# Kernel tuning notes

Measured on AMD Instinct MI355X. Metric: run time of the kernel, lower is better.

Reference implementation:

```python
import jax, jax.numpy as jnp
import numpy as np

# ---- problem dims ----
B, S, C, H, W = 4, 8, 3, 256, 256
P = 68          # keypoints (self.points)
DS = 4          # detector downsample
WIN = 8
STEPS = 10      # Gauss-Newton iterations per frame pair
EPS = 1e-6
GRAY_W = jnp.array([0.299, 0.587, 0.114], dtype=jnp.float32)

# window offsets [K,2] in (x,y)
_rng = jnp.arange(-WIN, WIN + 1, dtype=jnp.float32)
_OFF = jnp.stack(jnp.meshgrid(_rng, _rng, indexing='xy'), -1).reshape(-1, 2)


def setup_inputs() -> dict:
    key = jax.random.key(0)
    k1, k2 = jax.random.split(key)
    inputs = jax.random.normal(k1, (B, S, C, H, W), dtype=jnp.float32)
    Wdet = jax.random.normal(k2, (P, C, 3, 3), dtype=jnp.float32) * 0.1
    bdet = jnp.zeros((P,), dtype=jnp.float32)
    return {"inputs": inputs, "Wdet": Wdet, "bdet": bdet}


def _bilinear(img, xy):
    # img [H,W]; xy [...,2] in (x,y) pixel coords -> sampled values [...]
    x = jnp.clip(xy[..., 0], 0.0, W - 1.001)
    y = jnp.clip(xy[..., 1], 0.0, H - 1.001)
    x0 = jnp.floor(x); y0 = jnp.floor(y)
    wx = x - x0; wy = y - y0
    x0i = x0.astype(jnp.int32); y0i = y0.astype(jnp.int32)
    x1i = jnp.minimum(x0i + 1, W - 1); y1i = jnp.minimum(y0i + 1, H - 1)
    v00 = img[y0i, x0i]; v01 = img[y0i, x1i]
    v10 = img[y1i, x0i]; v11 = img[y1i, x1i]
    return (1 - wy) * ((1 - wx) * v00 + wx * v01) + wy * ((1 - wx) * v10 + wx * v11)


def _grad_xy(img):
    # central differences with edge replication
    px = jnp.pad(img, ((0, 0), (1, 1)), mode='edge')
    py = jnp.pad(img, ((1, 1), (0, 0)), mode='edge')
    gx = (px[:, 2:] - px[:, :-2]) * 0.5
    gy = (py[2:, :] - py[:-2, :]) * 0.5
    return gx, gy


def _lk_track(old, new, pts):
    # one Lucas-Kanade tracking step: old/new [H,W] gray, pts [P,2] -> [P,2]
    gx, gy = _grad_xy(old)
    pos0 = pts[:, None, :] + _OFF[None]            # [P,K,2]
    I0 = _bilinear(old, pos0)                      # [P,K] template patch
    Ix = _bilinear(gx, pos0)
    Iy = _bilinear(gy, pos0)
    Gxx = (Ix * Ix).sum(-1); Gxy = (Ix * Iy).sum(-1); Gyy = (Iy * Iy).sum(-1)
    det = Gxx * Gyy - Gxy * Gxy + EPS
    Ginv = jnp.stack([jnp.stack([Gyy, -Gxy], -1),
                      jnp.stack([-Gxy, Gxx], -1)], -2) / det[:, None, None]  # [P,2,2]

    def step(i, v):
        I1 = _bilinear(new, pos0 + v[:, None, :])  # [P,K]
        err = I0 - I1
        b = jnp.stack([(err * Ix).sum(-1), (err * Iy).sum(-1)], -1)  # [P,2]
        return v + jnp.einsum('pij,pj->pi', Ginv, b)

    v = jax.lax.fori_loop(0, STEPS, step, jnp.zeros_like(pts))
    return pts + v


def _lk_forward_backward(gray, locs):
    # gray [S,H,W], locs [S,P,2] -> nextPts, fbackPts, backPts each [S,P,2]
    def f(pts, frames):
        o, n = frames
        q = _lk_track(o, n, pts)
        return q, q

    # forward: track detector locs of frame 0 through the sequence
    _, fout = jax.lax.scan(f, locs[0], (gray[:-1], gray[1:]))
    nextPts = jnp.concatenate([locs[:1], fout], 0)
    ro, rn = gray[1:][::-1], gray[:-1][::-1]
    # forward-backward: track the forward end point back to frame 0
    _, fbout = jax.lax.scan(f, nextPts[-1], (ro, rn))
    fbackPts = jnp.concatenate([nextPts[-1:], fbout], 0)[::-1]
    # backward: track detector locs of last frame back through the sequence
    _, bout = jax.lax.scan(f, locs[-1], (ro, rn))
    backPts = jnp.concatenate([locs[-1:], bout], 0)[::-1]
    return nextPts, fbackPts, backPts


def _detector(x, Wdet, bdet):
    # x [N,C,H,W] -> heatmaps [N,P,H/DS,W/DS], locs [N,P,2] (pixel coords), scores [N,P]
    hm = jax.lax.conv_general_dilated(
        x, Wdet, window_strides=(DS, DS), padding='SAME',
        dimension_numbers=('NCHW', 'OIHW', 'NCHW')) + bdet[None, :, None, None]
    N, _, Hd, Wd = hm.shape
    flat = hm.reshape(N, P, Hd * Wd)
    prob = jax.nn.softmax(flat, axis=-1)
    ys, xs = jnp.meshgrid(jnp.arange(Hd, dtype=hm.dtype),
                          jnp.arange(Wd, dtype=hm.dtype), indexing='ij')
    ex = (prob * xs.reshape(-1)).sum(-1) * DS   # soft-argmax, upscaled to input px
    ey = (prob * ys.reshape(-1)).sum(-1) * DS
    locs = jnp.stack([ex, ey], -1)
    scos = flat.max(-1)
    return hm, locs, scos


def reference(inputs, Wdet, bdet):
    x = inputs.reshape(B * S, C, H, W)
    hm, locs, scos = _detector(x, Wdet, bdet)
    heatmaps = hm.reshape(B, S, P, H // DS, W // DS)
    batch_locs = locs.reshape(B, S, P, 2)
    batch_scos = scos.reshape(B, S, P)
    gray = jnp.einsum('bschw,c->bshw', inputs, GRAY_W)  # [B,S,H,W]
    nextPts, fbackPts, backPts = jax.vmap(_lk_forward_backward)(gray, batch_locs)
    return heatmaps, batch_locs, batch_scos, nextPts, fbackPts, backPts
```

## Files before the change

### kernel.cpp

```cpp
#include <hip/hip_runtime.h>
#include <math.h>

namespace {
constexpr int Bn = 4, Sn = 8, Cn = 3, Himg = 256, Wimg = 256;
constexpr int Pn = 68, DS = 4, WIN = 8, STEPS = 10;
constexpr int HWi = Himg * Wimg;
constexpr int NIMG = Bn * Sn;
constexpr int HD = Himg / DS, WD = Wimg / DS;
constexpr int Kwin = (2 * WIN + 1) * (2 * WIN + 1);
}

__global__ __launch_bounds__(256) void gray2_kernel(const float* __restrict__ in,
                                                    float* __restrict__ gray,
                                                    float* __restrict__ sh) {
    int idx = blockIdx.x * blockDim.x + threadIdx.x;
    int total = NIMG * HWi / 4;
    if (idx >= total) return;
    int img = idx / (HWi / 4);
    int off = idx % (HWi / 4);
    const float* base = in + (size_t)img * 3 * HWi;
    float4 c0 = ((const float4*)(base))[off];
    float4 c1 = ((const float4*)(base + HWi))[off];
    float4 c2 = ((const float4*)(base + 2 * HWi))[off];
    float4 g;
    g.x = 0.299f * c0.x + 0.587f * c1.x + 0.114f * c2.x;
    g.y = 0.299f * c0.y + 0.587f * c1.y + 0.114f * c2.y;
    g.z = 0.299f * c0.z + 0.587f * c1.z + 0.114f * c2.z;
    g.w = 0.299f * c0.w + 0.587f * c1.w + 0.114f * c2.w;
    float gn = 0.f;
    int gi = idx * 4 + 4;
    if (gi < NIMG * HWi) {
        int i2 = gi / HWi;
        int o2 = gi % HWi;
        const float* b2 = in + (size_t)i2 * 3 * HWi;
        gn = 0.299f * b2[o2] + 0.587f * b2[o2 + HWi] + 0.114f * b2[o2 + 2 * HWi];
    }
    ((float4*)(gray + (size_t)img * HWi))[off] = g;
    float4 s;
    s.x = g.y; s.y = g.z; s.z = g.w; s.w = gn;
    ((float4*)(sh + (size_t)img * HWi))[off] = s;
}

__global__ __launch_bounds__(256) void conv_kernel(const float* __restrict__ x,
                                                   const float* __restrict__ Wdet,
                                                   const float* __restrict__ bdet,
                                                   float* __restrict__ hm) {
    __shared__ float wsh[Pn * 27];
    __shared__ float bsh[Pn];
    __shared__ float insh[3][3][Wimg];
    int n = blockIdx.x >> 6;
    int oy = blockIdx.x & 63;
    int tid = threadIdx.x;
    for (int t = tid; t < Pn * 27; t += 256) wsh[t] = Wdet[t];
    if (tid < Pn) bsh[tid] = bdet[tid];
    for (int t = tid; t < 3 * 3 * Wimg; t += 256) {
        int c = t / (3 * Wimg);
        int r = (t / Wimg) % 3;
        int col = t % Wimg;
        insh[c][r][col] = x[(size_t)n * 3 * HWi + (size_t)c * HWi + (oy * 4 + r) * Wimg + col];
    }
    __syncthreads();
    int ox = tid & 63;
    int wid = tid >> 6;
    float in_reg[27];
    #pragma unroll
    for (int c = 0; c < 3; c++)
        #pragma unroll
        for (int ky = 0; ky < 3; ky++)
            #pragma unroll
            for (int kx = 0; kx < 3; kx++)
                in_reg[c * 9 + ky * 3 + kx] = insh[c][ky][ox * 4 + kx];
    #pragma unroll
    for (int i = 0; i < 17; i++) {
        int p = wid + i * 4;
        const float* w = &wsh[p * 27];
        float acc = bsh[p];
        #pragma unroll
        for (int j = 0; j < 27; j++) acc += w[j] * in_reg[j];
        hm[(size_t)n * Pn * 4096 + (size_t)p * 4096 + oy * 64 + ox] = acc;
    }
}

__global__ __launch_bounds__(256) void smax_kernel(const float* __restrict__ hm,
                                                   float* __restrict__ locs,
                                                   float* __restrict__ scos) {
    int row = blockIdx.x;
    const float4* r = (const float4*)(hm + (size_t)row * 4096);
    int tid = threadIdx.x;
    float v[16];
    #pragma unroll
    for (int j = 0; j < 4; j++) {
        float4 q = r[tid + 256 * j];
        v[4 * j + 0] = q.x; v[4 * j + 1] = q.y; v[4 * j + 2] = q.z; v[4 * j + 3] = q.w;
    }
    float m = v[0];
    #pragma unroll
    for (int i = 1; i < 16; i++) m = fmaxf(m, v[i]);
    __shared__ float redm[4];
    #pragma unroll
    for (int o = 32; o; o >>= 1) m = fmaxf(m, __shfl_xor(m, o, 64));
    int wid = tid >> 6, lane = tid & 63;
    if (lane == 0) redm[wid] = m;
    __syncthreads();
    m = fmaxf(fmaxf(redm[0], redm[1]), fmaxf(redm[2], redm[3]));
    float s = 0.f, sx = 0.f, sy = 0.f;
    #pragma unroll
    for (int j = 0; j < 4; j++) {
        #pragma unroll
        for (int q = 0; q < 4; q++) {
            int e = (tid + 256 * j) * 4 + q;
            float ev = expf(v[4 * j + q] - m);
            s += ev;
            sx += ev * (float)(e & 63);
            sy += ev * (float)(e >> 6);
        }
    }
    #pragma unroll
    for (int o = 32; o; o >>= 1) {
        s  += __shfl_xor(s, o, 64);
        sx += __shfl_xor(sx, o, 64);
        sy += __shfl_xor(sy, o, 64);
    }
    __shared__ float reds[3][4];
    if (lane == 0) { reds[0][wid] = s; reds[1][wid] = sx; reds[2][wid] = sy; }
    __syncthreads();
    if (tid == 0) {
        float S_ = reds[0][0] + reds[0][1] + reds[0][2] + reds[0][3];
        float SX = reds[1][0] + reds[1][1] + reds[1][2] + reds[1][3];
        float SY = reds[2][0] + reds[2][1] + reds[2][2] + reds[2][3];
        locs[(size_t)row * 2 + 0] = SX / S_ * 4.0f;
        locs[(size_t)row * 2 + 1] = SY / S_ * 4.0f;
        scos[row] = m;
    }
}

template <int CTRL>
__device__ inline float dpp_add(float v) {
    int t = __builtin_amdgcn_update_dpp(0, __builtin_bit_cast(int, v), CTRL, 0xF, 0xF, true);
    return v + __builtin_bit_cast(float, t);
}

__device__ inline float wredw(float v) {
    v = dpp_add<0x111>(v);
    v = dpp_add<0x112>(v);
    v = dpp_add<0x114>(v);
    v = dpp_add<0x118>(v);
    v = dpp_add<0x142>(v);
    v = dpp_add<0x143>(v);
    int s = __builtin_amdgcn_readlane(__builtin_bit_cast(int, v), 63);
    return __builtin_bit_cast(float, s);
}

__device__ void lk_track_pair(const float* __restrict__ oldI, const float* __restrict__ oldS,
                              const float* __restrict__ newI, const float* __restrict__ newS,
                              float& px, float& py, const float* dxs, const float* dys,
                              float s4w) {
    const float XM = (float)(Wimg - 1.001);
    const float YM = (float)(Himg - 1.001);
    float I0[5], Ix[5], Iy[5], qx[5], qy[5];
    {
        float wx[5], wy[5];
        const float* pb[5];
        int xe[5], am[5], a0[5], a1[5], ap[5], xm[5], xp[5];
        #pragma unroll
        for (int j = 0; j < 5; j++) {
            qx[j] = px + dxs[j];
            qy[j] = py + dys[j];
            float x = fminf(fmaxf(qx[j], 0.0f), XM);
            float y = fminf(fmaxf(qy[j], 0.0f), YM);
            float x0f = floorf(x), y0f = floorf(y);
            wx[j] = x - x0f; wy[j] = y - y0f;
            int xi = (int)x0f, yi = (int)y0f;
            xe[j] = xi & ~1;
            pb[j] = (xi & 1) ? oldS : oldI;
            xm[j] = max(xi - 1, 0);
            xp[j] = min(xi + 2, Wimg - 1);
            a0[j] = yi * Wimg;
            a1[j] = a0[j] + Wimg;
            am[j] = max(yi - 1, 0) * Wimg;
            ap[j] = min(yi + 2, Himg - 1) * Wimg;
        }
        float2 Pm[5], P0[5], P1[5], Pp[5];
        float c0m[5], c0p[5], c1m[5], c1p[5];
        #pragma unroll
        for (int j = 0; j < 5; j++) {
            Pm[j] = *(const float2*)(pb[j] + am[j] + xe[j]);
            P0[j] = *(const float2*)(pb[j] + a0[j] + xe[j]);
            P1[j] = *(const float2*)(pb[j] + a1[j] + xe[j]);
            Pp[j] = *(const float2*)(pb[j] + ap[j] + xe[j]);
            c0m[j] = oldI[a0[j] + xm[j]];
            c0p[j] = oldI[a0[j] + xp[j]];
            c1m[j] = oldI[a1[j] + xm[j]];
            c1p[j] = oldI[a1[j] + xp[j]];
        }
        #pragma unroll
        for (int j = 0; j < 5; j++) {
            float m0 = Pm[j].x, m1 = Pm[j].y;
            float c00 = P0[j].x, c01 = P0[j].y;
            float c10 = P1[j].x, c11 = P1[j].y;
            float p0 = Pp[j].x, p1 = Pp[j].y;
            float u = 1.0f - wx[j], t = 1.0f - wy[j];
            I0[j] = t * (u * c00 + wx[j] * c01) + wy[j] * (u * c10 + wx[j] * c11);
            float gx00 = 0.5f * (c01 - c0m[j]);
            float gx01 = 0.5f * (c0p[j] - c00);
            float gx10 = 0.5f * (c11 - c1m[j]);
            float gx11 = 0.5f * (c1p[j] - c10);
            Ix[j] = t * (u * gx00 + wx[j] * gx01) + wy[j] * (u * gx10 + wx[j] * gx11);
            float gy00 = 0.5f * (c10 - m0);
            float gy01 = 0.5f * (c11 - m1);
            float gy10 = 0.5f * (p0 - c00);
            float gy11 = 0.5f * (p1 - c01);
            Iy[j] = t * (u * gy00 + wx[j] * gy01) + wy[j] * (u * gy10 + wx[j] * gy11);
        }
        Ix[4] *= s4w;
        Iy[4] *= s4w;
    }
    float gxx = 0.f, gxy = 0.f, gyy = 0.f;
    #pragma unroll
    for (int j = 0; j < 5; j++) { gxx += Ix[j] * Ix[j]; gxy += Ix[j] * Iy[j]; gyy += Iy[j] * Iy[j]; }
    gxx = wredw(gxx); gxy = wredw(gxy); gyy = wredw(gyy);
    float det = gxx * gyy - gxy * gxy + 1e-6f;
    float A = gyy / det, Bv = -gxy / det, D = gxx / det;
    float vx = 0.f, vy = 0.f;
    for (int it = 0; it < STEPS; ++it) {
        float fx[5], fy[5];
        const float* pb[5];
        int aa[5];
        #pragma unroll
        for (int j = 0; j < 5; j++) {
            float x = fminf(fmaxf(qx[j] + vx, 0.0f), XM);
            float y = fminf(fmaxf(qy[j] + vy, 0.0f), YM);
            float x0f = floorf(x), y0f = floorf(y);
            fx[j] = x - x0f; fy[j] = y - y0f;
            int xi = (int)x0f, yi = (int)y0f;
            pb[j] = (xi & 1) ? newS : newI;
            aa[j] = yi * Wimg + (xi & ~1);
        }
        float2 R0[5], R1[5];
        #pragma unroll
        for (int j = 0; j < 5; j++) {
            R0[j] = *(const float2*)(pb[j] + aa[j]);
            R1[j] = *(const float2*)(pb[j] + aa[j] + Wimg);
        }
        float bx = 0.f, by = 0.f;
        #pragma unroll
        for (int j = 0; j < 5; j++) {
            float u = 1.0f - fx[j], t = 1.0f - fy[j];
            float I1 = t * (u * R0[j].x + fx[j] * R0[j].y) + fy[j] * (u * R1[j].x + fx[j] * R1[j].y);
            float err = I0[j] - I1;
            bx += err * Ix[j];
            by += err * Iy[j];
        }
        bx = wredw(bx); by = wredw(by);
        vx += A * bx + Bv * by;
        vy += Bv * bx + D * by;
    }
    px += vx; py += vy;
}

__global__ __launch_bounds__(64) void lk_pair_kernel(const float* __restrict__ gray,
                                                     const float* __restrict__ sh,
                                                     const float* __restrict__ locs,
                                                     float* __restrict__ nextPts,
                                                     float* __restrict__ fbackPts,
                                                     float* __restrict__ backPts) {
    int g = blockIdx.x;
    int typ = g / (Bn * Pn);
    int r = g % (Bn * Pn);
    int b = r / Pn;
    int p = r % Pn;
    int lane = threadIdx.x;
    const float* G = gray + (size_t)b * Sn * HWi;
    const float* S = sh + (size_t)b * Sn * HWi;
    float dxs[5], dys[5];
    #pragma unroll
    for (int j = 0; j < 4; j++) {
        int k = lane + 64 * j;
        dxs[j] = (float)(k % 17 - 8);
        dys[j] = (float)(k / 17 - 8);
    }
    {
        int k4 = (lane < Kwin - 256) ? 256 + lane : 256;
        dxs[4] = (float)(k4 % 17 - 8);
        dys[4] = (float)(k4 / 17 - 8);
    }
    float s4w = (lane < Kwin - 256) ? 1.0f : 0.0f;
    auto LIDX = [&](int s) { return (((size_t)b * Sn + s) * Pn + p) * 2; };
    if (typ == 0) {
        float px = locs[LIDX(0)], py = locs[LIDX(0) + 1];
        if (lane == 0) { nextPts[LIDX(0)] = px; nextPts[LIDX(0) + 1] = py; }
        for (int s = 0; s < 7; s++) {
            lk_track_pair(G + s * HWi, S + s * HWi, G + (s + 1) * HWi, S + (s + 1) * HWi,
                          px, py, dxs, dys, s4w);
            if (lane == 0) { nextPts[LIDX(s + 1)] = px; nextPts[LIDX(s + 1) + 1] = py; }
        }
        if (lane == 0) { fbackPts[LIDX(7)] = px; fbackPts[LIDX(7) + 1] = py; }
        for (int i = 0; i < 7; i++) {
            lk_track_pair(G + (7 - i) * HWi, S + (7 - i) * HWi, G + (6 - i) * HWi, S + (6 - i) * HWi,
                          px, py, dxs, dys, s4w);
            if (lane == 0) { fbackPts[LIDX(6 - i)] = px; fbackPts[LIDX(6 - i) + 1] = py; }
        }
    } else {
        float px = locs[LIDX(7)], py = locs[LIDX(7) + 1];
        if (lane == 0) { backPts[LIDX(7)] = px; backPts[LIDX(7) + 1] = py; }
        for (int i = 0; i < 7; i++) {
            lk_track_pair(G + (7 - i) * HWi, S + (7 - i) * HWi, G + (6 - i) * HWi, S + (6 - i) * HWi,
                          px, py, dxs, dys, s4w);
            if (lane == 0) { backPts[LIDX(6 - i)] = px; backPts[LIDX(6 - i) + 1] = py; }
        }
    }
}

__device__ inline float px_fly(const float* __restrict__ im, int idx) {
    return 0.299f * im[idx] + 0.587f * im[idx + HWi] + 0.114f * im[idx + 2 * HWi];
}

__device__ void lk_track_fly(const float* __restrict__ oldI, const float* __restrict__ newI,
                             float& px, float& py, const float* dxs, const float* dys,
                             float s4w) {
    const float XM = (float)(Wimg - 1.001);
    const float YM = (float)(Himg - 1.001);
    float I0[5], Ix[5], Iy[5], qx[5], qy[5];
    {
        float wx[5], wy[5];
        int am[5], a0[5], a1[5], ap[5], xm[5], x0[5], x1[5], xp[5];
        #pragma unroll
        for (int j = 0; j < 5; j++) {
            qx[j] = px + dxs[j]; qy[j] = py + dys[j];
            float x = fminf(fmaxf(qx[j], 0.0f), XM);
            float y = fminf(fmaxf(qy[j], 0.0f), YM);
            float x0f = floorf(x), y0f = floorf(y);
            wx[j] = x - x0f; wy[j] = y - y0f;
            int xi = (int)x0f, yi = (int)y0f;
            x0[j] = xi; x1[j] = min(xi + 1, Wimg - 1);
            xm[j] = max(xi - 1, 0); xp[j] = min(xi + 2, Wimg - 1);
            a0[j] = yi * Wimg;
            a1[j] = min(yi + 1, Himg - 1) * Wimg;
            am[j] = max(yi - 1, 0) * Wimg;
            ap[j] = min(yi + 2, Himg - 1) * Wimg;
        }
        #pragma unroll
        for (int j = 0; j < 5; j++) {
            float m0 = px_fly(oldI, am[j] + x0[j]), m1 = px_fly(oldI, am[j] + x1[j]);
            float c0m = px_fly(oldI, a0[j] + xm[j]), c00 = px_fly(oldI, a0[j] + x0[j]);
            float c01 = px_fly(oldI, a0[j] + x1[j]), c0p = px_fly(oldI, a0[j] + xp[j]);
            float c1m = px_fly(oldI, a1[j] + xm[j]), c10 = px_fly(oldI, a1[j] + x0[j]);
            float c11 = px_fly(oldI, a1[j] + x1[j]), c1p = px_fly(oldI, a1[j] + xp[j]);
            float p0 = px_fly(oldI, ap[j] + x0[j]), p1 = px_fly(oldI, ap[j] + x1[j]);
            float u = 1.0f - wx[j], t = 1.0f - wy[j];
            I0[j] = t * (u * c00 + wx[j] * c01) + wy[j] * (u * c10 + wx[j] * c11);
            Ix[j] = t * (u * 0.5f * (c01 - c0m) + wx[j] * 0.5f * (c0p - c00))
                  + wy[j] * (u * 0.5f * (c11 - c1m) + wx[j] * 0.5f * (c1p - c10));
            Iy[j] = t * (u * 0.5f * (c10 - m0) + wx[j] * 0.5f * (c11 - m1))
                  + wy[j] * (u * 0.5f * (p0 - c00) + wx[j] * 0.5f * (p1 - c01));
        }
        Ix[4] *= s4w; Iy[4] *= s4w;
    }
    float gxx = 0.f, gxy = 0.f, gyy = 0.f;
    #pragma unroll
    for (int j = 0; j < 5; j++) { gxx += Ix[j] * Ix[j]; gxy += Ix[j] * Iy[j]; gyy += Iy[j] * Iy[j]; }
    gxx = wredw(gxx); gxy = wredw(gxy); gyy = wredw(gyy);
    float det = gxx * gyy - gxy * gxy + 1e-6f;
    float A = gyy / det, Bv = -gxy / det, D = gxx / det;
    float vx = 0.f, vy = 0.f;
    for (int it = 0; it < STEPS; ++it) {
        float bx = 0.f, by = 0.f;
        #pragma unroll
        for (int j = 0; j < 5; j++) {
            float x = fminf(fmaxf(qx[j] + vx, 0.0f), XM);
            float y = fminf(fmaxf(qy[j] + vy, 0.0f), YM);
            float x0f = floorf(x), y0f = floorf(y);
            float fxx = x - x0f, fyy = y - y0f;
            int xi = (int)x0f, yi = (int)y0f;
            int ad = yi * Wimg + xi;
            float v00 = px_fly(newI, ad), v01 = px_fly(newI, ad + 1);
            float v10 = px_fly(newI, ad + Wimg), v11 = px_fly(newI, ad + Wimg + 1);
            float u = 1.0f - fxx, t = 1.0f - fyy;
            float I1 = t * (u * v00 + fxx * v01) + fyy * (u * v10 + fxx * v11);
            float err = I0[j] - I1;
            bx += err * Ix[j];
            by += err * Iy[j];
        }
        bx = wredw(bx); by = wredw(by);
        vx += A * bx + Bv * by;
        vy += Bv * bx + D * by;
    }
    px += vx; py += vy;
}

__global__ __launch_bounds__(64) void lk_fly_kernel(const float* __restrict__ in,
                                                    const float* __restrict__ locs,
                                                    float* __restrict__ nextPts,
                                                    float* __restrict__ fbackPts,
                                                    float* __restrict__ backPts) {
    constexpr size_t FS = (size_t)3 * HWi;
    int g = blockIdx.x;
    int typ = g / (Bn * Pn);
    int r = g % (Bn * Pn);
    int b = r / Pn;
    int p = r % Pn;
    int lane = threadIdx.x;
    const float* G = in + (size_t)b * Sn * FS;
    float dxs[5], dys[5];
    #pragma unroll
    for (int j = 0; j < 4; j++) {
        int k = lane + 64 * j;
        dxs[j] = (float)(k % 17 - 8);
        dys[j] = (float)(k / 17 - 8);
    }
    {
        int k4 = (lane < Kwin - 256) ? 256 + lane : 256;
        dxs[4] = (float)(k4 % 17 - 8);
        dys[4] = (float)(k4 / 17 - 8);
    }
    float s4w = (lane < Kwin - 256) ? 1.0f : 0.0f;
    auto LIDX = [&](int s) { return (((size_t)b * Sn + s) * Pn + p) * 2; };
    if (typ == 0) {
        float px = locs[LIDX(0)], py = locs[LIDX(0) + 1];
        if (lane == 0) { nextPts[LIDX(0)] = px; nextPts[LIDX(0) + 1] = py; }
        for (int s = 0; s < 7; s++) {
            lk_track_fly(G + s * FS, G + (s + 1) * FS, px, py, dxs, dys, s4w);
            if (lane == 0) { nextPts[LIDX(s + 1)] = px; nextPts[LIDX(s + 1) + 1] = py; }
        }
        if (lane == 0) { fbackPts[LIDX(7)] = px; fbackPts[LIDX(7) + 1] = py; }
        for (int i = 0; i < 7; i++) {
            lk_track_fly(G + (7 - i) * FS, G + (6 - i) * FS, px, py, dxs, dys, s4w);
            if (lane == 0) { fbackPts[LIDX(6 - i)] = px; fbackPts[LIDX(6 - i) + 1] = py; }
        }
    } else {
        float px = locs[LIDX(7)], py = locs[LIDX(7) + 1];
        if (lane == 0) { backPts[LIDX(7)] = px; backPts[LIDX(7) + 1] = py; }
        for (int i = 0; i < 7; i++) {
            lk_track_fly(G + (7 - i) * FS, G + (6 - i) * FS, px, py, dxs, dys, s4w);
            if (lane == 0) { backPts[LIDX(6 - i)] = px; backPts[LIDX(6 - i) + 1] = py; }
        }
    }
}

extern "C" void kernel_launch(void* const* d_in, const int* in_sizes, int n_in,
                              void* d_out, int out_size, void* d_ws, size_t ws_size,
                              hipStream_t stream) {
    const float* inputs = (const float*)d_in[0];
    const float* Wdet = (const float*)d_in[1];
    const float* bdet = (const float*)d_in[2];
    float* out = (float*)d_out;

    const size_t N_hm = (size_t)Bn * Sn * Pn * HD * WD;
    const size_t N_pts = (size_t)Bn * Sn * Pn * 2;
    float* hm = out;
    float* locs = out + N_hm;
    float* scos = locs + N_pts;
    float* nextPts = scos + (size_t)Bn * Sn * Pn;
    float* fbackPts = nextPts + N_pts;
    float* backPts = fbackPts + N_pts;

    conv_kernel<<<NIMG * 64, 256, 0, stream>>>(inputs, Wdet, bdet, hm);
    smax_kernel<<<NIMG * Pn, 256, 0, stream>>>(hm, locs, scos);

    const size_t gray_elems = (size_t)NIMG * HWi;
    if (ws_size >= 2 * gray_elems * sizeof(float)) {
        float* gray = (float*)d_ws;
        float* sh = gray + gray_elems;
        gray2_kernel<<<(NIMG * HWi / 4 + 255) / 256, 256, 0, stream>>>(inputs, gray, sh);
        lk_pair_kernel<<<2 * Bn * Pn, 64, 0, stream>>>(gray, sh, locs, nextPts, fbackPts, backPts);
    } else {
        lk_fly_kernel<<<2 * Bn * Pn, 64, 0, stream>>>(inputs, locs, nextPts, fbackPts, backPts);
    }
}
```

Baseline: 121.7 us.

## Fuse grayscale into conv kernel and store quad-packed float4 bilinear layout

Removes the separate gray conversion kernel by computing grayscale rows inside the convolution kernel from the shared-memory input tile. The kernel writes a quad layout where each float4 holds the 2x2 bilinear neighbourhood, so each LK sample is one 16-byte load instead of two float2 loads chosen by parity. The first iteration reuses the template-time fetch of the new frame. This costs a larger workspace (4x the gray size) and more write traffic from the conv kernel, and the fly fallback gains edge-clamp fixes.

```diff
diff --git a/kernel.cpp b/kernel.cpp
--- a/kernel.cpp
+++ b/kernel.cpp
@@ -8,37 +8,76 @@
 constexpr int NIMG = Bn * Sn;
 constexpr int HD = Himg / DS, WD = Wimg / DS;
 constexpr int Kwin = (2 * WIN + 1) * (2 * WIN + 1);
-}
-
-__global__ __launch_bounds__(256) void gray2_kernel(const float* __restrict__ in,
-                                                    float* __restrict__ gray,
-                                                    float* __restrict__ sh) {
-    int idx = blockIdx.x * blockDim.x + threadIdx.x;
-    int total = NIMG * HWi / 4;
-    if (idx >= total) return;
-    int img = idx / (HWi / 4);
-    int off = idx % (HWi / 4);
-    const float* base = in + (size_t)img * 3 * HWi;
-    float4 c0 = ((const float4*)(base))[off];
-    float4 c1 = ((const float4*)(base + HWi))[off];
-    float4 c2 = ((const float4*)(base + 2 * HWi))[off];
-    float4 g;
-    g.x = 0.299f * c0.x + 0.587f * c1.x + 0.114f * c2.x;
-    g.y = 0.299f * c0.y + 0.587f * c1.y + 0.114f * c2.y;
-    g.z = 0.299f * c0.z + 0.587f * c1.z + 0.114f * c2.z;
-    g.w = 0.299f * c0.w + 0.587f * c1.w + 0.114f * c2.w;
-    float gn = 0.f;
-    int gi = idx * 4 + 4;
-    if (gi < NIMG * HWi) {
-        int i2 = gi / HWi;
-        int o2 = gi % HWi;
-        const float* b2 = in + (size_t)i2 * 3 * HWi;
-        gn = 0.299f * b2[o2] + 0.587f * b2[o2 + HWi] + 0.114f * b2[o2 + 2 * HWi];
-    }
-    ((float4*)(gray + (size_t)img * HWi))[off] = g;
-    float4 s;
-    s.x = g.y; s.y = g.z; s.z = g.w; s.w = gn;
-    ((float4*)(sh + (size_t)img * HWi))[off] = s;
+constexpr int QROWS = 257;
+constexpr int QFR = QROWS * 256;
+}
+
+__global__ __launch_bounds__(256) void mega_kernel(const float* __restrict__ x,
+                                                   const float* __restrict__ Wdet,
+                                                   const float* __restrict__ bdet,
+                                                   float* __restrict__ hm,
+                                                   float4* __restrict__ Q) {
+    __shared__ float wsh[Pn * 27];
+    __shared__ float bsh[Pn];
+    __shared__ float insh[3][5][Wimg];
+    __shared__ float grow[5][257];
+    int n = blockIdx.x >> 6;
+    int oy = blockIdx.x & 63;
+    int tid = threadIdx.x;
+    for (int t = tid; t < Pn * 27; t += 256) wsh[t] = Wdet[t];
+    if (tid < Pn) bsh[tid] = bdet[tid];
+    for (int t = tid; t < 3 * 5 * Wimg; t += 256) {
+        int c = t / (5 * Wimg);
+        int rem = t % (5 * Wimg);
+        int r = rem / Wimg;
+        int col = rem % Wimg;
+        int gr = min(max(4 * oy - 1 + r, 0), 255);
+        insh[c][r][col] = x[(size_t)n * 3 * HWi + (size_t)c * HWi + gr * Wimg + col];
+    }
+    __syncthreads();
+    int ox = tid & 63;
+    int wid = tid >> 6;
+    float in_reg[27];
+    #pragma unroll
+    for (int c = 0; c < 3; c++)
+        #pragma unroll
+        for (int ky = 0; ky < 3; ky++)
+            #pragma unroll
+            for (int kx = 0; kx < 3; kx++)
+                in_reg[c * 9 + ky * 3 + kx] = insh[c][1 + ky][ox * 4 + kx];
+    #pragma unroll
+    for (int i = 0; i < 17; i++) {
+        int p = wid + i * 4;
+        const float* w = &wsh[p * 27];
+        float acc = bsh[p];
+        #pragma unroll
+        for (int j = 0; j < 27; j++) acc += w[j] * in_reg[j];
+        hm[(size_t)n * Pn * 4096 + (size_t)p * 4096 + oy * 64 + ox] = acc;
+    }
+    #pragma unroll
+    for (int r = 0; r < 5; r++)
+        grow[r][tid] = 0.299f * insh[0][r][tid] + 0.587f * insh[1][r][tid] + 0.114f * insh[2][r][tid];
+    if (tid < 5) grow[tid][256] = grow[tid][255];
+    __syncthreads();
+    float4* qf = Q + (size_t)n * QFR;
+    #pragma unroll
+    for (int j = 0; j < 4; j++) {
+        int k = 4 * oy + j;
+        float4 q;
+        q.x = grow[j][tid];
+        q.y = grow[j + 1][tid];
+        q.z = grow[j][tid + 1];
+        q.w = grow[j + 1][tid + 1];
+        qf[k * 256 + tid] = q;
+    }
+    if (oy == 63) {
+        float4 q;
+        q.x = grow[4][tid];
+        q.y = grow[4][tid];
+        q.z = grow[4][tid + 1];
+        q.w = grow[4][tid + 1];
+        qf[256 * 256 + tid] = q;
+    }
 }
 
 __global__ __launch_bounds__(256) void conv_kernel(const float* __restrict__ x,
@@ -151,60 +190,51 @@
     return __builtin_bit_cast(float, s);
 }
 
-__device__ void lk_track_pair(const float* __restrict__ oldI, const float* __restrict__ oldS,
-                              const float* __restrict__ newI, const float* __restrict__ newS,
-                              float& px, float& py, const float* dxs, const float* dys,
-                              float s4w) {
+__device__ void lk_track_q(const float4* __restrict__ Qo, const float4* __restrict__ Qn,
+                           float& px, float& py, const float* dxs, const float* dys,
+                           float s4w) {
     const float XM = (float)(Wimg - 1.001);
     const float YM = (float)(Himg - 1.001);
     float I0[5], Ix[5], Iy[5], qx[5], qy[5];
+    float wx[5], wy[5];
+    float4 Q0[5];
     {
-        float wx[5], wy[5];
-        const float* pb[5];
-        int xe[5], am[5], a0[5], a1[5], ap[5], xm[5], xp[5];
+        int idA[5], idS[5], xm[5], xp[5];
         #pragma unroll
         for (int j = 0; j < 5; j++) {
             qx[j] = px + dxs[j];
             qy[j] = py + dys[j];
             float x = fminf(fmaxf(qx[j], 0.0f), XM);
             float y = fminf(fmaxf(qy[j], 0.0f), YM);
-            float x0f = floorf(x), y0f = floorf(y);
-            wx[j] = x - x0f; wy[j] = y - y0f;
-            int xi = (int)x0f, yi = (int)y0f;
-            xe[j] = xi & ~1;
-            pb[j] = (xi & 1) ? oldS : oldI;
+            float xf = floorf(x), yf = floorf(y);
+            wx[j] = x - xf; wy[j] = y - yf;
+            int xi = (int)xf, yi = (int)yf;
+            idA[j] = yi * 256 + xi;
+            idS[j] = (yi + 1) * 256;
             xm[j] = max(xi - 1, 0);
             xp[j] = min(xi + 2, Wimg - 1);
-            a0[j] = yi * Wimg;
-            a1[j] = a0[j] + Wimg;
-            am[j] = max(yi - 1, 0) * Wimg;
-            ap[j] = min(yi + 2, Himg - 1) * Wimg;
-        }
-        float2 Pm[5], P0[5], P1[5], Pp[5];
-        float c0m[5], c0p[5], c1m[5], c1p[5];
-        #pragma unroll
-        for (int j = 0; j < 5; j++) {
-            Pm[j] = *(const float2*)(pb[j] + am[j] + xe[j]);
-            P0[j] = *(const float2*)(pb[j] + a0[j] + xe[j]);
-            P1[j] = *(const float2*)(pb[j] + a1[j] + xe[j]);
-            Pp[j] = *(const float2*)(pb[j] + ap[j] + xe[j]);
-            c0m[j] = oldI[a0[j] + xm[j]];
-            c0p[j] = oldI[a0[j] + xp[j]];
-            c1m[j] = oldI[a1[j] + xm[j]];
-            c1p[j] = oldI[a1[j] + xp[j]];
-        }
-        #pragma unroll
-        for (int j = 0; j < 5; j++) {
-            float m0 = Pm[j].x, m1 = Pm[j].y;
-            float c00 = P0[j].x, c01 = P0[j].y;
-            float c10 = P1[j].x, c11 = P1[j].y;
-            float p0 = Pp[j].x, p1 = Pp[j].y;
+        }
+        float4 A[5], B[5];
+        float2 S1[5], S2[5];
+        #pragma unroll
+        for (int j = 0; j < 5; j++) {
+            A[j] = Qo[idA[j]];
+            B[j] = Qo[idA[j] + 512];
+            S1[j] = *reinterpret_cast<const float2*>(Qo + idS[j] + xm[j]);
+            S2[j] = *reinterpret_cast<const float2*>(Qo + idS[j] + xp[j]);
+            Q0[j] = Qn[idA[j] + 256];
+        }
+        #pragma unroll
+        for (int j = 0; j < 5; j++) {
+            float m0 = A[j].x, c00 = A[j].y, m1 = A[j].z, c01 = A[j].w;
+            float c10 = B[j].x, p0 = B[j].y, c11 = B[j].z, p1 = B[j].w;
+            float c0m = S1[j].x, c1m = S1[j].y, c0p = S2[j].x, c1p = S2[j].y;
             float u = 1.0f - wx[j], t = 1.0f - wy[j];
             I0[j] = t * (u * c00 + wx[j] * c01) + wy[j] * (u * c10 + wx[j] * c11);
-            float gx00 = 0.5f * (c01 - c0m[j]);
-            float gx01 = 0.5f * (c0p[j] - c00);
-            float gx10 = 0.5f * (c11 - c1m[j]);
-            float gx11 = 0.5f * (c1p[j] - c10);
+            float gx00 = 0.5f * (c01 - c0m);
+            float gx01 = 0.5f * (c0p - c00);
+            float gx10 = 0.5f * (c11 - c1m);
+            float gx11 = 0.5f * (c1p - c10);
             Ix[j] = t * (u * gx00 + wx[j] * gx01) + wy[j] * (u * gx10 + wx[j] * gx11);
             float gy00 = 0.5f * (c10 - m0);
             float gy01 = 0.5f * (c11 - m1);
@@ -222,31 +252,12 @@
     float det = gxx * gyy - gxy * gxy + 1e-6f;
     float A = gyy / det, Bv = -gxy / det, D = gxx / det;
     float vx = 0.f, vy = 0.f;
-    for (int it = 0; it < STEPS; ++it) {
-        float fx[5], fy[5];
-        const float* pb[5];
-        int aa[5];
-        #pragma unroll
-        for (int j = 0; j < 5; j++) {
-            float x = fminf(fmaxf(qx[j] + vx, 0.0f), XM);
-            float y = fminf(fmaxf(qy[j] + vy, 0.0f), YM);
-            float x0f = floorf(x), y0f = floorf(y);
-            fx[j] = x - x0f; fy[j] = y - y0f;
-            int xi = (int)x0f, yi = (int)y0f;
-            pb[j] = (xi & 1) ? newS : newI;
-            aa[j] = yi * Wimg + (xi & ~1);
-        }
-        float2 R0[5], R1[5];
-        #pragma unroll
-        for (int j = 0; j < 5; j++) {
-            R0[j] = *(const float2*)(pb[j] + aa[j]);
-            R1[j] = *(const float2*)(pb[j] + aa[j] + Wimg);
-        }
+    {
         float bx = 0.f, by = 0.f;
         #pragma unroll
         for (int j = 0; j < 5; j++) {
-            float u = 1.0f - fx[j], t = 1.0f - fy[j];
-            float I1 = t * (u * R0[j].x + fx[j] * R0[j].y) + fy[j] * (u * R1[j].x + fx[j] * R1[j].y);
+            float u = 1.0f - wx[j], t = 1.0f - wy[j];
+            float I1 = t * (u * Q0[j].x + wx[j] * Q0[j].z) + wy[j] * (u * Q0[j].y + wx[j] * Q0[j].w);
             float err = I0[j] - I1;
             bx += err * Ix[j];
             by += err * Iy[j];
@@ -255,23 +266,49 @@
         vx += A * bx + Bv * by;
         vy += Bv * bx + D * by;
     }
+    for (int it = 1; it < STEPS; ++it) {
+        float fx[5], fy[5];
+        int id[5];
+        #pragma unroll
+        for (int j = 0; j < 5; j++) {
+            float x = fminf(fmaxf(qx[j] + vx, 0.0f), XM);
+            float y = fminf(fmaxf(qy[j] + vy, 0.0f), YM);
+            float xf = floorf(x), yf = floorf(y);
+            fx[j] = x - xf; fy[j] = y - yf;
+            int xi = (int)xf, yi = (int)yf;
+            id[j] = (yi + 1) * 256 + xi;
+        }
+        float4 Qv[5];
+        #pragma unroll
+        for (int j = 0; j < 5; j++) Qv[j] = Qn[id[j]];
+        float bx = 0.f, by = 0.f;
+        #pragma unroll
+        for (int j = 0; j < 5; j++) {
+            float u = 1.0f - fx[j], t = 1.0f - fy[j];
+            float I1 = t * (u * Qv[j].x + fx[j] * Qv[j].z) + fy[j] * (u * Qv[j].y + fx[j] * Qv[j].w);
+            float err = I0[j] - I1;
+            bx += err * Ix[j];
+            by += err * Iy[j];
+        }
+        bx = wredw(bx); by = wredw(by);
+        vx += A * bx + Bv * by;
+        vy += Bv * bx + D * by;
+    }
     px += vx; py += vy;
 }
 
-__global__ __launch_bounds__(64) void lk_pair_kernel(const float* __restrict__ gray,
-                                                     const float* __restrict__ sh,
-                                                     const float* __restrict__ locs,
-                                                     float* __restrict__ nextPts,
-                                                     float* __restrict__ fbackPts,
-                                                     float* __restrict__ backPts) {
+__global__ __launch_bounds__(64) void lk_q_kernel(const float4* __restrict__ Q,
+                                                  const float* __restrict__ locs,
+                                                  float* __restrict__ nextPts,
+                                                  float* __restrict__ fbackPts,
+                                                  float* __restrict__ backPts) {
     int g = blockIdx.x;
     int typ = g / (Bn * Pn);
     int r = g % (Bn * Pn);
     int b = r / Pn;
     int p = r % Pn;
     int lane = threadIdx.x;
-    const float* G = gray + (size_t)b * Sn * HWi;
-    const float* S = sh + (size_t)b * Sn * HWi;
+    const float4* F = Q + (size_t)b * Sn * QFR;
     float dxs[5], dys[5];
     #pragma unroll
     for (int j = 0; j < 4; j++) {
@@ -290,22 +327,19 @@
         float px = locs[LIDX(0)], py = locs[LIDX(0) + 1];
         if (lane == 0) { nextPts[LIDX(0)] = px; nextPts[LIDX(0) + 1] = py; }
         for (int s = 0; s < 7; s++) {
-            lk_track_pair(G + s * HWi, S + s * HWi, G + (s + 1) * HWi, S + (s + 1) * HWi,
-                          px, py, dxs, dys, s4w);
+            lk_track_q(F + s * QFR, F + (s + 1) * QFR, px, py, dxs, dys, s4w);
             if (lane == 0) { nextPts[LIDX(s + 1)] = px; nextPts[LIDX(s + 1) + 1] = py; }
         }
         if (lane == 0) { fbackPts[LIDX(7)] = px; fbackPts[LIDX(7) + 1] = py; }
         for (int i = 0; i < 7; i++) {
-            lk_track_pair(G + (7 - i) * HWi, S + (7 - i) * HWi, G + (6 - i) * HWi, S + (6 - i) * HWi,
-                          px, py, dxs, dys, s4w);
+            lk_track_q(F + (7 - i) * QFR, F + (6 - i) * QFR, px, py, dxs, dys, s4w);
             if (lane == 0) { fbackPts[LIDX(6 - i)] = px; fbackPts[LIDX(6 - i) + 1] = py; }
         }
     } else {
         float px = locs[LIDX(7)], py = locs[LIDX(7) + 1];
         if (lane == 0) { backPts[LIDX(7)] = px; backPts[LIDX(7) + 1] = py; }
         for (int i = 0; i < 7; i++) {
-            lk_track_pair(G + (7 - i) * HWi, S + (7 - i) * HWi, G + (6 - i) * HWi, S + (6 - i) * HWi,
-                          px, py, dxs, dys, s4w);
+            lk_track_q(F + (7 - i) * QFR, F + (6 - i) * QFR, px, py, dxs, dys, s4w);
             if (lane == 0) { backPts[LIDX(6 - i)] = px; backPts[LIDX(6 - i) + 1] = py; }
         }
     }
@@ -373,8 +407,10 @@
             float fxx = x - x0f, fyy = y - y0f;
             int xi = (int)x0f, yi = (int)y0f;
             int ad = yi * Wimg + xi;
-            float v00 = px_fly(newI, ad), v01 = px_fly(newI, ad + 1);
-            float v10 = px_fly(newI, ad + Wimg), v11 = px_fly(newI, ad + Wimg + 1);
+            int d1 = (xi < Wimg - 1) ? 1 : 0;
+            int d2 = (yi < Himg - 1) ? Wimg : 0;
+            float v00 = px_fly(newI, ad), v01 = px_fly(newI, ad + d1);
+            float v10 = px_fly(newI, ad + d2), v11 = px_fly(newI, ad + d2 + d1);
             float u = 1.0f - fxx, t = 1.0f - fyy;
             float I1 = t * (u * v00 + fxx * v01) + fyy * (u * v10 + fxx * v11);
             float err = I0[j] - I1;
@@ -454,16 +490,15 @@
     float* fbackPts = nextPts + N_pts;
     float* backPts = fbackPts + N_pts;
 
-    conv_kernel<<<NIMG * 64, 256, 0, stream>>>(inputs, Wdet, bdet, hm);
-    smax_kernel<<<NIMG * Pn, 256, 0, stream>>>(hm, locs, scos);
-
-    const size_t gray_elems = (size_t)NIMG * HWi;
-    if (ws_size >= 2 * gray_elems * sizeof(float)) {
-        float* gray = (float*)d_ws;
-        float* sh = gray + gray_elems;
-        gray2_kernel<<<(NIMG * HWi / 4 + 255) / 256, 256, 0, stream>>>(inputs, gray, sh);
-        lk_pair_kernel<<<2 * Bn * Pn, 64, 0, stream>>>(gray, sh, locs, nextPts, fbackPts, backPts);
+    const size_t q_bytes = (size_t)NIMG * QFR * sizeof(float4);
+    if (ws_size >= q_bytes) {
+        float4* Q = (float4*)d_ws;
+        mega_kernel<<<NIMG * 64, 256, 0, stream>>>(inputs, Wdet, bdet, hm, Q);
+        smax_kernel<<<NIMG * Pn, 256, 0, stream>>>(hm, locs, scos);
+        lk_q_kernel<<<2 * Bn * Pn, 64, 0, stream>>>(Q, locs, nextPts, fbackPts, backPts);
     } else {
+        conv_kernel<<<NIMG * 64, 256, 0, stream>>>(inputs, Wdet, bdet, hm);
+        smax_kernel<<<NIMG * Pn, 256, 0, stream>>>(hm, locs, scos);
         lk_fly_kernel<<<2 * Bn * Pn, 64, 0, stream>>>(inputs, locs, nextPts, fbackPts, backPts);
     }
 }
```

Result: faster. 111.4 us (-8.5%).
